# Kernel tuning notes

Hardware: AMD Instinct MI355X
Metric: run time of the kernel (lower is better)

The kernel has to match this reference:

```python
import jax, jax.numpy as jnp
import numpy as np

H = 8  # n_heads
NEG = -1e32
LN_EPS = 1e-5


def setup_inputs() -> dict:
    key = jax.random.key(0)
    ks = jax.random.split(key, 10)
    B, S, D = 8, 1024, 512
    sd = 1.0 / np.sqrt(D)
    return {
        "q_in": jax.random.normal(ks[0], (B, S, D), jnp.float32),
        "k_in": jax.random.normal(ks[1], (B, S, D), jnp.float32),
        "v_in": jax.random.normal(ks[2], (B, S, D), jnp.float32),
        "state_mask": jax.random.randint(ks[3], (B, S, S), 0, 2, jnp.int32),
        "Wq": jax.random.normal(ks[4], (D, D), jnp.float32) * sd,
        "bq": jnp.zeros((D,), jnp.float32),
        "Wv": jax.random.normal(ks[5], (D, D), jnp.float32) * sd,
        "bv": jnp.zeros((D,), jnp.float32),
        "Wo": jax.random.normal(ks[6], (D, D), jnp.float32) * sd,
        "bo": jnp.zeros((D,), jnp.float32),
        "gammas": jax.random.normal(ks[7], (H, 1, 1), jnp.float32) * 0.1,
        "ln_g": jnp.ones((D,), jnp.float32),
        "ln_b": jnp.zeros((D,), jnp.float32),
    }


def _heads(x, B, S, h, dk):
    # [B,S,D] -> [B,h,S,dk]
    return x.reshape(B, S, h, dk).transpose(0, 2, 1, 3)


def reference(q_in, k_in, v_in, state_mask, Wq, bq, Wv, bv, Wo, bo, gammas, ln_g, ln_b):
    B, S, D = q_in.shape
    dk = D // H
    # strict causal mask (tril(-1)), as in DTransformerLayer with peek_cur=False
    causal = jnp.tril(jnp.ones((S, S), bool), -1)[None, None]  # [1,1,S,S]

    # --- LrState: decay-gamma scores on RAW embeddings, scaled by sqrt(d_model) (source quirk) ---
    qh = _heads(q_in, B, S, H, dk)
    kh = _heads(k_in, B, S, H, dk)
    s_scores = jnp.einsum("bhqd,bhkd->bhqk", qh, kh) / jnp.sqrt(jnp.float32(D))
    total_effect = jnp.clip(jnp.exp(-jax.nn.softplus(gammas)), 1e-5, 1e5)[None]  # [1,H,1,1]
    s_scores = s_scores * total_effect
    new_mask = (state_mask[:, None] != 0) & causal  # cluster mask AND causal
    s_scores = jnp.where(new_mask, s_scores, 0.0)

    # --- MultiHeadAttention (kq_same=True: k uses q_linear) ---
    q = _heads(q_in @ Wq + bq, B, S, H, dk)
    k = _heads(k_in @ Wq + bq, B, S, H, dk)
    v = _heads(v_in @ Wv + bv, B, S, H, dk)
    scores = jnp.einsum("bhqd,bhkd->bhqk", q, k) / jnp.sqrt(jnp.float32(dk))
    scores = jnp.where(causal, scores, NEG)
    scores = scores + s_scores
    scores = jnp.where(causal, scores, NEG)
    probs = jax.nn.softmax(scores, axis=-1)
    probs = jnp.where(causal, probs, 0.0)
    o = jnp.einsum("bhqk,bhkd->bhqd", probs, v)
    o = o.transpose(0, 2, 1, 3).reshape(B, S, D) @ Wo + bo

    # residual (dropout inactive in eval) + LayerNorm
    x = q_in + o
    mu = jnp.mean(x, -1, keepdims=True)
    var = jnp.mean(jnp.square(x - mu), -1, keepdims=True)
    return (x - mu) * jax.lax.rsqrt(var + LN_EPS) * ln_g + ln_b
```

## Files before the change

### kernel.cpp

```cpp
#include <hip/hip_runtime.h>
#include <math.h>

#define S_LEN 1024
#define D_MOD 512
#define NH 8
#define DK 64
#define NB 8

typedef __attribute__((ext_vector_type(8))) short short8;
typedef __attribute__((ext_vector_type(4))) float floatx4;

union U8 { ushort u[8]; short8 v; };

__device__ __forceinline__ ushort f2bf(float x) {
  unsigned u = __float_as_uint(x);
  unsigned r = (u + 0x7fffu + ((u >> 16) & 1u)) >> 16;
  return (ushort)r;
}

__global__ __launch_bounds__(256) void prep_kern(
    const float* __restrict__ q, const float* __restrict__ k,
    const float* __restrict__ v, const int* __restrict__ smask,
    ushort* __restrict__ qo, ushort* __restrict__ ko,
    ushort* __restrict__ vo, unsigned long long* __restrict__ mb)
{
  const int y = blockIdx.y;
  const int t = threadIdx.x;
  if (y < 3) {
    const float* src = (y == 0) ? q : (y == 1) ? k : v;
    ushort* dst = (y == 0) ? qo : (y == 1) ? ko : vo;
    const int i = blockIdx.x * 256 + t;
    const float4 a = *((const float4*)src + i * 2);
    const float4 b = *((const float4*)src + i * 2 + 1);
    U8 o;
    o.u[0] = f2bf(a.x); o.u[1] = f2bf(a.y); o.u[2] = f2bf(a.z); o.u[3] = f2bf(a.w);
    o.u[4] = f2bf(b.x); o.u[5] = f2bf(b.y); o.u[6] = f2bf(b.z); o.u[7] = f2bf(b.w);
    *(short8*)(dst + (size_t)i * 8) = o.v;
  } else {
    const int row = blockIdx.x * 4 + (t >> 6);
    const int lane = t & 63;
    const int* p = smask + (size_t)row * S_LEN;
    unsigned long long mine = 0;
#pragma unroll
    for (int r = 0; r < 16; ++r) {
      int m = p[r * 64 + lane];
      unsigned long long w = __ballot(m != 0);
      if (lane == r) mine = w;
    }
    if (lane < 16) mb[(size_t)row * 16 + lane] = mine;
  }
}

__global__ __launch_bounds__(256) void wtrans3_kern(
    const float* __restrict__ W0, const float* __restrict__ W1,
    const float* __restrict__ W2, ushort* __restrict__ T0,
    ushort* __restrict__ T1, ushort* __restrict__ T2)
{
  const int z = blockIdx.z;
  const float* W = (z == 0) ? W0 : (z == 1) ? W1 : W2;
  ushort* Wt = (z == 0) ? T0 : (z == 1) ? T1 : T2;
  __shared__ __align__(16) ushort tile[64][72];
  const int t = threadIdx.x;
  const int n0 = blockIdx.x * 64;
  const int k0 = blockIdx.y * 64;
  {
    const int r = t >> 2;
    const int c0 = (t & 3) * 16;
    const float* p = &W[(size_t)(k0 + r) * 512 + n0 + c0];
#pragma unroll
    for (int j = 0; j < 16; ++j) tile[r][c0 + j] = f2bf(p[j]);
  }
  __syncthreads();
  {
    const int c = t >> 2;
    const int kg = (t & 3) * 16;
    U8 lo, hi;
#pragma unroll
    for (int j = 0; j < 8; ++j) lo.u[j] = tile[kg + j][c];
#pragma unroll
    for (int j = 0; j < 8; ++j) hi.u[j] = tile[kg + 8 + j][c];
    ushort* q = &Wt[(size_t)(n0 + c) * 512 + k0 + kg];
    *(short8*)q = lo.v;
    *(short8*)(q + 8) = hi.v;
  }
}

__global__ __launch_bounds__(256) void gemm_qkv_kern(
    const ushort* __restrict__ qr, const ushort* __restrict__ kr,
    const ushort* __restrict__ vr, const ushort* __restrict__ Wqt,
    const ushort* __restrict__ Wvt, const float* __restrict__ bq,
    const float* __restrict__ bv, ushort* __restrict__ Qo,
    ushort* __restrict__ Ko, ushort* __restrict__ VtO)
{
  __shared__ __align__(16) ushort Bl[2][64][64];

  const int z = blockIdx.z;
  const ushort* A = (z == 0) ? qr : (z == 1) ? kr : vr;
  const ushort* Wt = (z == 2) ? Wvt : Wqt;
  const float* bias = (z == 2) ? bv : bq;

  const int t = threadIdx.x;
  const int w = t >> 6;
  const int lane = t & 63;
  const int quad = lane >> 4;
  const int i16 = lane & 15;
  const int mbase = blockIdx.x * 128 + w * 32;
  const int nbase = blockIdx.y * 64;

  const int sr = t >> 2;
  const int slc = (t & 3) * 2;
  const int sp0 = ((slc ^ (sr & 7)) * 8);
  const int sp1 = (((slc + 1) ^ (sr & 7)) * 8);
  const ushort* Bg = Wt + (size_t)(nbase + sr) * 512 + (t & 3) * 16;
  const int xb = i16 & 7;

  const ushort* Ap = A + (size_t)(mbase + i16) * 512 + quad * 8;

  floatx4 acc[2][4];
#pragma unroll
  for (int mi = 0; mi < 2; ++mi)
#pragma unroll
    for (int ni = 0; ni < 4; ++ni) acc[mi][ni] = (floatx4)(0.f);

  short8 areg[3][2][2];
#pragma unroll
  for (int d = 0; d < 2; ++d)
#pragma unroll
    for (int mi = 0; mi < 2; ++mi)
#pragma unroll
      for (int kc = 0; kc < 2; ++kc)
        areg[d][mi][kc] = *(const short8*)(Ap + d * 64 + kc * 32 + mi * 16 * 512);

  {
    short8 b0 = *(const short8*)Bg;
    short8 b1 = *(const short8*)(Bg + 8);
    *(short8*)&Bl[0][sr][sp0] = b0;
    *(short8*)&Bl[0][sr][sp1] = b1;
    __syncthreads();
  }

#pragma unroll
  for (int kt = 0; kt < 8; ++kt) {
    const int cb = kt & 1;
    short8 nb0, nb1;
    if (kt < 7) {
      nb0 = *(const short8*)(Bg + (kt + 1) * 64);
      nb1 = *(const short8*)(Bg + (kt + 1) * 64 + 8);
    }
    if (kt < 6) {
#pragma unroll
      for (int mi = 0; mi < 2; ++mi)
#pragma unroll
        for (int kc = 0; kc < 2; ++kc)
          areg[(kt + 2) % 3][mi][kc] =
              *(const short8*)(Ap + (kt + 2) * 64 + kc * 32 + mi * 16 * 512);
    }
    short8 bf[2][4];
#pragma unroll
    for (int kc = 0; kc < 2; ++kc)
#pragma unroll
      for (int ni = 0; ni < 4; ++ni)
        bf[kc][ni] = *(const short8*)&Bl[cb][ni * 16 + i16][((kc * 4 + quad) ^ xb) * 8];
#pragma unroll
    for (int kc = 0; kc < 2; ++kc)
#pragma unroll
      for (int mi = 0; mi < 2; ++mi)
#pragma unroll
        for (int ni = 0; ni < 4; ++ni)
          acc[mi][ni] = __builtin_amdgcn_mfma_f32_16x16x32_bf16(
              areg[kt % 3][mi][kc], bf[kc][ni], acc[mi][ni], 0, 0, 0);
    if (kt < 7) {
      *(short8*)&Bl[cb ^ 1][sr][sp0] = nb0;
      *(short8*)&Bl[cb ^ 1][sr][sp1] = nb1;
      __syncthreads();
    }
  }

  float bv4[4];
#pragma unroll
  for (int ni = 0; ni < 4; ++ni) bv4[ni] = bias[nbase + ni * 16 + i16];

  if (z < 2) {
    ushort* C = (z == 0) ? Qo : Ko;
#pragma unroll
    for (int mi = 0; mi < 2; ++mi)
#pragma unroll
      for (int ni = 0; ni < 4; ++ni)
#pragma unroll
        for (int r = 0; r < 4; ++r) {
          const int m = mbase + mi * 16 + quad * 4 + r;
          const int n = nbase + ni * 16 + i16;
          C[(size_t)m * 512 + n] = f2bf(acc[mi][ni][r] + bv4[ni]);
        }
  } else {
#pragma unroll
    for (int mi = 0; mi < 2; ++mi)
#pragma unroll
      for (int ni = 0; ni < 4; ++ni) {
        const int m = mbase + mi * 16 + quad * 4;
        const int b = m >> 10;
        const int s = m & 1023;
        const int n = nbase + ni * 16 + i16;
        const int h = n >> 6;
        const int c = n & 63;
        ushort4 pk;
        pk.x = f2bf(acc[mi][ni][0] + bv4[ni]);
        pk.y = f2bf(acc[mi][ni][1] + bv4[ni]);
        pk.z = f2bf(acc[mi][ni][2] + bv4[ni]);
        pk.w = f2bf(acc[mi][ni][3] + bv4[ni]);
        *(ushort4*)(VtO + (((size_t)b * NH + h) * DK + c) * S_LEN + s) = pk;
      }
  }
}

__global__ __launch_bounds__(256) void gemm_out_kern(
    const ushort* __restrict__ A, const ushort* __restrict__ Wt,
    const float* __restrict__ bias, const float* __restrict__ R,
    float* __restrict__ X)
{
  __shared__ __align__(16) ushort Bl[2][64][64];

  const int t = threadIdx.x;
  const int w = t >> 6;
  const int lane = t & 63;
  const int quad = lane >> 4;
  const int i16 = lane & 15;
  const int mbase = blockIdx.x * 128 + w * 32;
  const int nbase = blockIdx.y * 64;

  const int sr = t >> 2;
  const int slc = (t & 3) * 2;
  const int sp0 = ((slc ^ (sr & 7)) * 8);
  const int sp1 = (((slc + 1) ^ (sr & 7)) * 8);
  const ushort* Bg = Wt + (size_t)(nbase + sr) * 512 + (t & 3) * 16;
  const int xb = i16 & 7;

  const ushort* Ap = A + (size_t)(mbase + i16) * 512 + quad * 8;

  floatx4 acc[2][4];
#pragma unroll
  for (int mi = 0; mi < 2; ++mi)
#pragma unroll
    for (int ni = 0; ni < 4; ++ni) acc[mi][ni] = (floatx4)(0.f);

  short8 areg[3][2][2];
#pragma unroll
  for (int d = 0; d < 2; ++d)
#pragma unroll
    for (int mi = 0; mi < 2; ++mi)
#pragma unroll
      for (int kc = 0; kc < 2; ++kc)
        areg[d][mi][kc] = *(const short8*)(Ap + d * 64 + kc * 32 + mi * 16 * 512);

  {
    short8 b0 = *(const short8*)Bg;
    short8 b1 = *(const short8*)(Bg + 8);
    *(short8*)&Bl[0][sr][sp0] = b0;
    *(short8*)&Bl[0][sr][sp1] = b1;
    __syncthreads();
  }

#pragma unroll
  for (int kt = 0; kt < 8; ++kt) {
    const int cb = kt & 1;
    short8 nb0, nb1;
    if (kt < 7) {
      nb0 = *(const short8*)(Bg + (kt + 1) * 64);
      nb1 = *(const short8*)(Bg + (kt + 1) * 64 + 8);
    }
    if (kt < 6) {
#pragma unroll
      for (int mi = 0; mi < 2; ++mi)
#pragma unroll
        for (int kc = 0; kc < 2; ++kc)
          areg[(kt + 2) % 3][mi][kc] =
              *(const short8*)(Ap + (kt + 2) * 64 + kc * 32 + mi * 16 * 512);
    }
    short8 bf[2][4];
#pragma unroll
    for (int kc = 0; kc < 2; ++kc)
#pragma unroll
      for (int ni = 0; ni < 4; ++ni)
        bf[kc][ni] = *(const short8*)&Bl[cb][ni * 16 + i16][((kc * 4 + quad) ^ xb) * 8];
#pragma unroll
    for (int kc = 0; kc < 2; ++kc)
#pragma unroll
      for (int mi = 0; mi < 2; ++mi)
#pragma unroll
        for (int ni = 0; ni < 4; ++ni)
          acc[mi][ni] = __builtin_amdgcn_mfma_f32_16x16x32_bf16(
              areg[kt % 3][mi][kc], bf[kc][ni], acc[mi][ni], 0, 0, 0);
    if (kt < 7) {
      *(short8*)&Bl[cb ^ 1][sr][sp0] = nb0;
      *(short8*)&Bl[cb ^ 1][sr][sp1] = nb1;
      __syncthreads();
    }
  }

  float bv4[4];
#pragma unroll
  for (int ni = 0; ni < 4; ++ni) bv4[ni] = bias[nbase + ni * 16 + i16];
#pragma unroll
  for (int mi = 0; mi < 2; ++mi)
#pragma unroll
    for (int ni = 0; ni < 4; ++ni)
#pragma unroll
      for (int r = 0; r < 4; ++r) {
        const int m = mbase + mi * 16 + quad * 4 + r;
        const int n = nbase + ni * 16 + i16;
        X[(size_t)m * 512 + n] = acc[mi][ni][r] + bv4[ni] + R[(size_t)m * 512 + n];
      }
}

__global__ __launch_bounds__(256) void attn_kern(
    const ushort* __restrict__ Qb, const ushort* __restrict__ Kb,
    const ushort* __restrict__ VtG, const ushort* __restrict__ qraw,
    const ushort* __restrict__ kraw,
    const unsigned long long* __restrict__ mbits,
    const float* __restrict__ gammas, ushort* __restrict__ Obf)
{
  __shared__ __align__(16) ushort Kp[2][64][64];
  __shared__ __align__(16) ushort Kr[2][64][64];
  __shared__ __align__(16) ushort Vc[2][64][64];
  __shared__ __align__(16) ushort Pl[4][16][64];

  const int t = threadIdx.x;
  const int w = t >> 6;
  const int lane = t & 63;
  const int quad = lane >> 4;
  const int i16 = lane & 15;
  const int bh = blockIdx.x;
  const int b = bh >> 3;
  const int h = bh & 7;
  const int p = blockIdx.y;

  const float gam = gammas[h];
  float te = __expf(-log1pf(__expf(gam)));
  te = fminf(fmaxf(te, 1e-5f), 1e5f);
  const float c1 = 0.125f * 1.44269504f;
  const float c2 = te * 0.044194173824159216f * 1.44269504f;

  const int xi = i16 & 7;
  const int rr = t >> 3;
  const int lc = t & 7;
  const int pc = ((lc ^ (rr & 7)) * 8);

  const ushort* kpgB = Kb + ((size_t)b * S_LEN + rr) * D_MOD + h * DK + lc * 8;
  const ushort* krgB = kraw + ((size_t)b * S_LEN + rr) * D_MOD + h * DK + lc * 8;
  const ushort* vgB  = VtG + ((size_t)bh * DK + rr) * S_LEN + lc * 8;

#pragma unroll
  for (int seg = 0; seg < 2; ++seg) {
    const int qt = seg ? (15 - p) : p;
    const int qbase = qt * 64 + w * 16;

    short8 Qp[2], Qr[2];
    {
      const ushort* qp = Qb + ((size_t)b * S_LEN + qbase + i16) * D_MOD + h * DK + quad * 8;
      const ushort* qq = qraw + ((size_t)b * S_LEN + qbase + i16) * D_MOD + h * DK + quad * 8;
#pragma unroll
      for (int s = 0; s < 2; ++s) {
        Qp[s] = *(const short8*)(qp + s * 32);
        Qr[s] = *(const short8*)(qq + s * 32);
      }
    }

    floatx4 Oacc[4];
#pragma unroll
    for (int t4 = 0; t4 < 4; ++t4) Oacc[t4] = (floatx4)(0.f);
    float l_run[4] = {0.f, 0.f, 0.f, 0.f};

    const int nit = qt + 1;

    {
      short8 k0v0 = *(const short8*)kpgB;
      short8 k0v1 = *(const short8*)(kpgB + 32 * D_MOD);
      short8 r0v0 = *(const short8*)krgB;
      short8 r0v1 = *(const short8*)(krgB + 32 * D_MOD);
      short8 v0v0 = *(const short8*)vgB;
      short8 v0v1 = *(const short8*)(vgB + 32 * S_LEN);
      __syncthreads();
      *(short8*)&Kp[0][rr][pc] = k0v0;
      *(short8*)&Kp[0][rr + 32][pc] = k0v1;
      *(short8*)&Kr[0][rr][pc] = r0v0;
      *(short8*)&Kr[0][rr + 32][pc] = r0v1;
      *(short8*)&Vc[0][rr][pc] = v0v0;
      *(short8*)&Vc[0][rr + 32][pc] = v0v1;
      __syncthreads();
    }

    for (int kt = 0; kt < nit; ++kt) {
      const int cb = kt & 1;
      const bool havenext = (kt + 1 < nit);
      const bool diag = (kt == qt);

      short8 nk0, nk1, nr0, nr1, nv0, nv1;
      if (havenext) {
        const size_t ko = (size_t)(kt + 1) * 64;
        nk0 = *(const short8*)(kpgB + ko * D_MOD);
        nk1 = *(const short8*)(kpgB + ko * D_MOD + 32 * D_MOD);
        nr0 = *(const short8*)(krgB + ko * D_MOD);
        nr1 = *(const short8*)(krgB + ko * D_MOD + 32 * D_MOD);
        nv0 = *(const short8*)(vgB + ko);
        nv1 = *(const short8*)(vgB + ko + 32 * S_LEN);
      }

      unsigned long long mw[4];
#pragma unroll
      for (int r = 0; r < 4; ++r)
        mw[r] = mbits[((size_t)b * S_LEN + qbase + quad * 4 + r) * 16 + kt];

      floatx4 accp[4], accr[4];
#pragma unroll
      for (int t4 = 0; t4 < 4; ++t4) { accp[t4] = (floatx4)(0.f); accr[t4] = (floatx4)(0.f); }
#pragma unroll
      for (int s = 0; s < 2; ++s) {
        const int co = ((s * 4 + quad) ^ xi) * 8;
        short8 kp4[4], kr4[4];
#pragma unroll
        for (int t4 = 0; t4 < 4; ++t4) kp4[t4] = *(const short8*)&Kp[cb][t4 * 16 + i16][co];
#pragma unroll
        for (int t4 = 0; t4 < 4; ++t4) kr4[t4] = *(const short8*)&Kr[cb][t4 * 16 + i16][co];
#pragma unroll
        for (int t4 = 0; t4 < 4; ++t4)
          accp[t4] = __builtin_amdgcn_mfma_f32_16x16x32_bf16(Qp[s], kp4[t4], accp[t4], 0, 0, 0);
#pragma unroll
        for (int t4 = 0; t4 < 4; ++t4)
          accr[t4] = __builtin_amdgcn_mfma_f32_16x16x32_bf16(Qr[s], kr4[t4], accr[t4], 0, 0, 0);
      }

      const int k0g = kt * 64;
#pragma unroll
      for (int r = 0; r < 4; ++r) {
        const int qg = qbase + quad * 4 + r;
        const int prow = quad * 4 + r;
#pragma unroll
        for (int t4 = 0; t4 < 4; ++t4) {
          const float bitf = ((mw[r] >> (t4 * 16 + i16)) & 1ULL) ? c2 : 0.f;
          const float sv = accp[t4][r] * c1 + accr[t4][r] * bitf;
          float pv = __builtin_amdgcn_exp2f(sv);
          if (diag) {
            const int kg = k0g + t4 * 16 + i16;
            pv = (kg < qg) ? pv : 0.f;
          }
          l_run[r] += pv;
          const int kc = t4 * 2 + (i16 >> 3);
          Pl[w][prow][((kc ^ (prow & 7)) * 8) + (i16 & 7)] =
              (ushort)(__float_as_uint(pv) >> 16);
        }
      }

#pragma unroll
      for (int s = 0; s < 2; ++s) {
        const int co = ((s * 4 + quad) ^ xi) * 8;
        short8 a = *(const short8*)&Pl[w][i16][co];
#pragma unroll
        for (int t4 = 0; t4 < 4; ++t4) {
          short8 bv8 = *(const short8*)&Vc[cb][t4 * 16 + i16][co];
          Oacc[t4] = __builtin_amdgcn_mfma_f32_16x16x32_bf16(a, bv8, Oacc[t4], 0, 0, 0);
        }
      }

      if (havenext) {
        *(short8*)&Kp[cb ^ 1][rr][pc] = nk0;
        *(short8*)&Kp[cb ^ 1][rr + 32][pc] = nk1;
        *(short8*)&Kr[cb ^ 1][rr][pc] = nr0;
        *(short8*)&Kr[cb ^ 1][rr + 32][pc] = nr1;
        *(short8*)&Vc[cb ^ 1][rr][pc] = nv0;
        *(short8*)&Vc[cb ^ 1][rr + 32][pc] = nv1;
        __syncthreads();
      }
    }

#pragma unroll
    for (int r = 0; r < 4; ++r) {
      float l = l_run[r];
#pragma unroll
      for (int off = 1; off < 16; off <<= 1) l += __shfl_xor(l, off);
      const float inv = (l > 0.f) ? 1.f / l : 0.f;
      ushort* orow = Obf + ((size_t)b * S_LEN + qbase + quad * 4 + r) * D_MOD + h * DK;
#pragma unroll
      for (int t4 = 0; t4 < 4; ++t4)
        orow[t4 * 16 + i16] = f2bf(Oacc[t4][r] * inv);
    }
  }
}

__global__ __launch_bounds__(256) void ln_kern(
    const float* __restrict__ X, const float* __restrict__ gw,
    const float* __restrict__ bw, float* __restrict__ out)
{
  const int row = blockIdx.x * 4 + (threadIdx.x >> 6);
  const int lane = threadIdx.x & 63;
  const int c = lane * 8;
  const float* xp = &X[(size_t)row * D_MOD + c];
  const float4 x0 = *(const float4*)xp;
  const float4 x1 = *(const float4*)(xp + 4);
  float xv[8] = {x0.x, x0.y, x0.z, x0.w, x1.x, x1.y, x1.z, x1.w};
  float sum = 0.f;
#pragma unroll
  for (int u = 0; u < 8; ++u) sum += xv[u];
#pragma unroll
  for (int off = 1; off < 64; off <<= 1) sum += __shfl_xor(sum, off, 64);
  const float mu = sum * (1.f / 512.f);
  float ss = 0.f;
#pragma unroll
  for (int u = 0; u < 8; ++u) { xv[u] -= mu; ss += xv[u] * xv[u]; }
#pragma unroll
  for (int off = 1; off < 64; off <<= 1) ss += __shfl_xor(ss, off, 64);
  const float rstd = rsqrtf(ss * (1.f / 512.f) + 1e-5f);
  const float4 g0 = *(const float4*)&gw[c];
  const float4 g1 = *(const float4*)&gw[c + 4];
  const float4 b0 = *(const float4*)&bw[c];
  const float4 b1 = *(const float4*)&bw[c + 4];
  float* op = &out[(size_t)row * D_MOD + c];
  *(float4*)op = make_float4(xv[0] * rstd * g0.x + b0.x,
                             xv[1] * rstd * g0.y + b0.y,
                             xv[2] * rstd * g0.z + b0.z,
                             xv[3] * rstd * g0.w + b0.w);
  *(float4*)(op + 4) = make_float4(xv[4] * rstd * g1.x + b1.x,
                                   xv[5] * rstd * g1.y + b1.y,
                                   xv[6] * rstd * g1.z + b1.z,
                                   xv[7] * rstd * g1.w + b1.w);
}

extern "C" void kernel_launch(void* const* d_in, const int* in_sizes, int n_in,
                              void* d_out, int out_size, void* d_ws, size_t ws_size,
                              hipStream_t stream)
{
  const float* q_in  = (const float*)d_in[0];
  const float* k_in  = (const float*)d_in[1];
  const float* v_in  = (const float*)d_in[2];
  const int*   smask = (const int*)d_in[3];
  const float* Wq = (const float*)d_in[4];
  const float* bq = (const float*)d_in[5];
  const float* Wv = (const float*)d_in[6];
  const float* bv = (const float*)d_in[7];
  const float* Wo = (const float*)d_in[8];
  const float* bo = (const float*)d_in[9];
  const float* gammas = (const float*)d_in[10];
  const float* ln_g = (const float*)d_in[11];
  const float* ln_b = (const float*)d_in[12];
  float* out = (float*)d_out;

  char* ws = (char*)d_ws;
  const size_t BF = (size_t)NB * S_LEN * D_MOD * sizeof(ushort);
  ushort* qr  = (ushort*)(ws);
  ushort* kr  = (ushort*)(ws + BF);
  ushort* vr  = (ushort*)(ws + 2 * BF);
  ushort* Obf = (ushort*)(ws + 2 * BF);
  ushort* Qbf = (ushort*)(ws + 3 * BF);
  ushort* Kbf = (ushort*)(ws + 4 * BF);
  ushort* Vt  = (ushort*)(ws + 5 * BF);
  unsigned long long* mbits = (unsigned long long*)(ws + 6 * BF);
  ushort* Wqt = (ushort*)(ws + 6 * BF + (1 << 20));
  ushort* Wvt = Wqt + 512 * 512;
  ushort* Wot = Wvt + 512 * 512;
  float*  X   = (float*)ws;

  const dim3 tb(256);

  prep_kern<<<dim3(2048, 4), tb, 0, stream>>>(q_in, k_in, v_in, smask,
                                              qr, kr, vr, mbits);
  wtrans3_kern<<<dim3(8, 8, 3), tb, 0, stream>>>(Wq, Wv, Wo, Wqt, Wvt, Wot);

  gemm_qkv_kern<<<dim3(64, 8, 3), tb, 0, stream>>>(qr, kr, vr, Wqt, Wvt,
                                                   bq, bv, Qbf, Kbf, Vt);

  attn_kern<<<dim3(64, 8), tb, 0, stream>>>(Qbf, Kbf, Vt, qr, kr, mbits,
                                            gammas, Obf);

  gemm_out_kern<<<dim3(64, 8), tb, 0, stream>>>(Obf, Wot, bo, q_in, X);
  ln_kern<<<2048, tb, 0, stream>>>(X, ln_g, ln_b, out);
}
```

Measured before the change: 231.2 us.

## Restructure attention to 32x32 MFMA with 2-wave blocks and fold weight transpose into prep

The attention kernel now uses 128-thread blocks where each wave handles 32 query rows. It computes the two score products with 32x32x16 bf16 MFMA in transposed (K x Q) form, which puts one query per lane, loads a single mask word per tile, and lets P be written as packed 4-element stores. The softmax scale factor is folded into the Q projection epilogue, and the weight-transpose kernel is merged into the prep kernel as an extra grid row, saving one launch. The tradeoffs are half as many waves per block and higher register pressure from the 16-wide accumulators.

```diff
diff --git a/kernel.cpp b/kernel.cpp
--- a/kernel.cpp
+++ b/kernel.cpp
@@ -9,6 +9,7 @@
 
 typedef __attribute__((ext_vector_type(8))) short short8;
 typedef __attribute__((ext_vector_type(4))) float floatx4;
+typedef __attribute__((ext_vector_type(16))) float floatx16;
 
 union U8 { ushort u[8]; short8 v; };
 
@@ -18,12 +19,18 @@
   return (ushort)r;
 }
 
+#define SC1 0.18033688f
+
 __global__ __launch_bounds__(256) void prep_kern(
     const float* __restrict__ q, const float* __restrict__ k,
     const float* __restrict__ v, const int* __restrict__ smask,
-    ushort* __restrict__ qo, ushort* __restrict__ ko,
-    ushort* __restrict__ vo, unsigned long long* __restrict__ mb)
+    const float* __restrict__ W0, const float* __restrict__ W1,
+    const float* __restrict__ W2,
+    ushort* __restrict__ qo, ushort* __restrict__ ko, ushort* __restrict__ vo,
+    unsigned long long* __restrict__ mb,
+    ushort* __restrict__ T0, ushort* __restrict__ T1, ushort* __restrict__ T2)
 {
+  __shared__ __align__(16) ushort tile[64][72];
   const int y = blockIdx.y;
   const int t = threadIdx.x;
   if (y < 3) {
@@ -36,7 +43,7 @@
     o.u[0] = f2bf(a.x); o.u[1] = f2bf(a.y); o.u[2] = f2bf(a.z); o.u[3] = f2bf(a.w);
     o.u[4] = f2bf(b.x); o.u[5] = f2bf(b.y); o.u[6] = f2bf(b.z); o.u[7] = f2bf(b.w);
     *(short8*)(dst + (size_t)i * 8) = o.v;
-  } else {
+  } else if (y == 3) {
     const int row = blockIdx.x * 4 + (t >> 6);
     const int lane = t & 63;
     const int* p = smask + (size_t)row * S_LEN;
@@ -48,40 +55,34 @@
       if (lane == r) mine = w;
     }
     if (lane < 16) mb[(size_t)row * 16 + lane] = mine;
-  }
-}
-
-__global__ __launch_bounds__(256) void wtrans3_kern(
-    const float* __restrict__ W0, const float* __restrict__ W1,
-    const float* __restrict__ W2, ushort* __restrict__ T0,
-    ushort* __restrict__ T1, ushort* __restrict__ T2)
-{
-  const int z = blockIdx.z;
-  const float* W = (z == 0) ? W0 : (z == 1) ? W1 : W2;
-  ushort* Wt = (z == 0) ? T0 : (z == 1) ? T1 : T2;
-  __shared__ __align__(16) ushort tile[64][72];
-  const int t = threadIdx.x;
-  const int n0 = blockIdx.x * 64;
-  const int k0 = blockIdx.y * 64;
-  {
-    const int r = t >> 2;
-    const int c0 = (t & 3) * 16;
-    const float* p = &W[(size_t)(k0 + r) * 512 + n0 + c0];
-#pragma unroll
-    for (int j = 0; j < 16; ++j) tile[r][c0 + j] = f2bf(p[j]);
-  }
-  __syncthreads();
-  {
-    const int c = t >> 2;
-    const int kg = (t & 3) * 16;
-    U8 lo, hi;
-#pragma unroll
-    for (int j = 0; j < 8; ++j) lo.u[j] = tile[kg + j][c];
-#pragma unroll
-    for (int j = 0; j < 8; ++j) hi.u[j] = tile[kg + 8 + j][c];
-    ushort* q = &Wt[(size_t)(n0 + c) * 512 + k0 + kg];
-    *(short8*)q = lo.v;
-    *(short8*)(q + 8) = hi.v;
+  } else {
+    if (blockIdx.x >= 192) return;
+    const int z = blockIdx.x / 64;
+    const int xy = blockIdx.x & 63;
+    const float* W = (z == 0) ? W0 : (z == 1) ? W1 : W2;
+    ushort* Wt = (z == 0) ? T0 : (z == 1) ? T1 : T2;
+    const int n0 = (xy & 7) * 64;
+    const int k0 = (xy >> 3) * 64;
+    {
+      const int r = t >> 2;
+      const int c0 = (t & 3) * 16;
+      const float* p = &W[(size_t)(k0 + r) * 512 + n0 + c0];
+#pragma unroll
+      for (int j = 0; j < 16; ++j) tile[r][c0 + j] = f2bf(p[j]);
+    }
+    __syncthreads();
+    {
+      const int c = t >> 2;
+      const int kg = (t & 3) * 16;
+      U8 lo, hi;
+#pragma unroll
+      for (int j = 0; j < 8; ++j) lo.u[j] = tile[kg + j][c];
+#pragma unroll
+      for (int j = 0; j < 8; ++j) hi.u[j] = tile[kg + 8 + j][c];
+      ushort* qd = &Wt[(size_t)(n0 + c) * 512 + k0 + kg];
+      *(short8*)qd = lo.v;
+      *(short8*)(qd + 8) = hi.v;
+    }
   }
 }
 
@@ -182,6 +183,7 @@
 
   if (z < 2) {
     ushort* C = (z == 0) ? Qo : Ko;
+    const float sc = (z == 0) ? SC1 : 1.f;
 #pragma unroll
     for (int mi = 0; mi < 2; ++mi)
 #pragma unroll
@@ -190,7 +192,7 @@
         for (int r = 0; r < 4; ++r) {
           const int m = mbase + mi * 16 + quad * 4 + r;
           const int n = nbase + ni * 16 + i16;
-          C[(size_t)m * 512 + n] = f2bf(acc[mi][ni][r] + bv4[ni]);
+          C[(size_t)m * 512 + n] = f2bf((acc[mi][ni][r] + bv4[ni]) * sc);
         }
   } else {
 #pragma unroll
@@ -312,7 +314,7 @@
       }
 }
 
-__global__ __launch_bounds__(256) void attn_kern(
+__global__ __launch_bounds__(128) void attn_kern(
     const ushort* __restrict__ Qb, const ushort* __restrict__ Kb,
     const ushort* __restrict__ VtG, const ushort* __restrict__ qraw,
     const ushort* __restrict__ kraw,
@@ -322,12 +324,14 @@
   __shared__ __align__(16) ushort Kp[2][64][64];
   __shared__ __align__(16) ushort Kr[2][64][64];
   __shared__ __align__(16) ushort Vc[2][64][64];
-  __shared__ __align__(16) ushort Pl[4][16][64];
+  __shared__ __align__(16) ushort Pl[2][32][64];
 
   const int t = threadIdx.x;
   const int w = t >> 6;
   const int lane = t & 63;
-  const int quad = lane >> 4;
+  const int l31 = lane & 31;
+  const int lh = lane >> 5;
+  const int quad = (lane >> 4) & 3;
   const int i16 = lane & 15;
   const int bh = blockIdx.x;
   const int b = bh >> 3;
@@ -337,55 +341,57 @@
   const float gam = gammas[h];
   float te = __expf(-log1pf(__expf(gam)));
   te = fminf(fmaxf(te, 1e-5f), 1e5f);
-  const float c1 = 0.125f * 1.44269504f;
   const float c2 = te * 0.044194173824159216f * 1.44269504f;
 
-  const int xi = i16 & 7;
-  const int rr = t >> 3;
+  const int rr4 = t >> 3;
   const int lc = t & 7;
-  const int pc = ((lc ^ (rr & 7)) * 8);
-
-  const ushort* kpgB = Kb + ((size_t)b * S_LEN + rr) * D_MOD + h * DK + lc * 8;
-  const ushort* krgB = kraw + ((size_t)b * S_LEN + rr) * D_MOD + h * DK + lc * 8;
-  const ushort* vgB  = VtG + ((size_t)bh * DK + rr) * S_LEN + lc * 8;
+  const int pc = ((lc ^ (rr4 & 7)) * 8);
+  const ushort* kpgB = Kb + ((size_t)b * S_LEN + rr4) * D_MOD + h * DK + lc * 8;
+  const ushort* krgB = kraw + ((size_t)b * S_LEN + rr4) * D_MOD + h * DK + lc * 8;
+  const ushort* vgB  = VtG + ((size_t)bh * DK + rr4) * S_LEN + lc * 8;
 
 #pragma unroll
   for (int seg = 0; seg < 2; ++seg) {
     const int qt = seg ? (15 - p) : p;
-    const int qbase = qt * 64 + w * 16;
-
-    short8 Qp[2], Qr[2];
+    const int qbase = qt * 64 + w * 32;
+    const int qg = qbase + l31;
+
+    short8 Qp[4], Qr[4];
     {
-      const ushort* qp = Qb + ((size_t)b * S_LEN + qbase + i16) * D_MOD + h * DK + quad * 8;
-      const ushort* qq = qraw + ((size_t)b * S_LEN + qbase + i16) * D_MOD + h * DK + quad * 8;
-#pragma unroll
-      for (int s = 0; s < 2; ++s) {
-        Qp[s] = *(const short8*)(qp + s * 32);
-        Qr[s] = *(const short8*)(qq + s * 32);
-      }
-    }
-
-    floatx4 Oacc[4];
-#pragma unroll
-    for (int t4 = 0; t4 < 4; ++t4) Oacc[t4] = (floatx4)(0.f);
-    float l_run[4] = {0.f, 0.f, 0.f, 0.f};
+      const ushort* qp = Qb + ((size_t)b * S_LEN + qg) * D_MOD + h * DK + lh * 8;
+      const ushort* qq = qraw + ((size_t)b * S_LEN + qg) * D_MOD + h * DK + lh * 8;
+#pragma unroll
+      for (int ds = 0; ds < 4; ++ds) {
+        Qp[ds] = *(const short8*)(qp + ds * 16);
+        Qr[ds] = *(const short8*)(qq + ds * 16);
+      }
+    }
+    const unsigned long long* mrow = mbits + ((size_t)b * S_LEN + qg) * 16;
+
+    floatx4 Oacc[2][4];
+#pragma unroll
+    for (int sub = 0; sub < 2; ++sub)
+#pragma unroll
+      for (int t4 = 0; t4 < 4; ++t4) Oacc[sub][t4] = (floatx4)(0.f);
+    float l_run = 0.f;
 
     const int nit = qt + 1;
 
     {
-      short8 k0v0 = *(const short8*)kpgB;
-      short8 k0v1 = *(const short8*)(kpgB + 32 * D_MOD);
-      short8 r0v0 = *(const short8*)krgB;
-      short8 r0v1 = *(const short8*)(krgB + 32 * D_MOD);
-      short8 v0v0 = *(const short8*)vgB;
-      short8 v0v1 = *(const short8*)(vgB + 32 * S_LEN);
+      short8 kv[4], rv[4], vv[4];
+#pragma unroll
+      for (int u = 0; u < 4; ++u) {
+        kv[u] = *(const short8*)(kpgB + (size_t)(16 * u) * D_MOD);
+        rv[u] = *(const short8*)(krgB + (size_t)(16 * u) * D_MOD);
+        vv[u] = *(const short8*)(vgB + (size_t)(16 * u) * S_LEN);
+      }
       __syncthreads();
-      *(short8*)&Kp[0][rr][pc] = k0v0;
-      *(short8*)&Kp[0][rr + 32][pc] = k0v1;
-      *(short8*)&Kr[0][rr][pc] = r0v0;
-      *(short8*)&Kr[0][rr + 32][pc] = r0v1;
-      *(short8*)&Vc[0][rr][pc] = v0v0;
-      *(short8*)&Vc[0][rr + 32][pc] = v0v1;
+#pragma unroll
+      for (int u = 0; u < 4; ++u) {
+        *(short8*)&Kp[0][rr4 + 16 * u][pc] = kv[u];
+        *(short8*)&Kr[0][rr4 + 16 * u][pc] = rv[u];
+        *(short8*)&Vc[0][rr4 + 16 * u][pc] = vv[u];
+      }
       __syncthreads();
     }
 
@@ -393,96 +399,105 @@
       const int cb = kt & 1;
       const bool havenext = (kt + 1 < nit);
       const bool diag = (kt == qt);
-
-      short8 nk0, nk1, nr0, nr1, nv0, nv1;
+      const int k0 = kt * 64;
+
+      short8 nk[4], nr[4], nv[4];
       if (havenext) {
-        const size_t ko = (size_t)(kt + 1) * 64;
-        nk0 = *(const short8*)(kpgB + ko * D_MOD);
-        nk1 = *(const short8*)(kpgB + ko * D_MOD + 32 * D_MOD);
-        nr0 = *(const short8*)(krgB + ko * D_MOD);
-        nr1 = *(const short8*)(krgB + ko * D_MOD + 32 * D_MOD);
-        nv0 = *(const short8*)(vgB + ko);
-        nv1 = *(const short8*)(vgB + ko + 32 * S_LEN);
-      }
-
-      unsigned long long mw[4];
-#pragma unroll
-      for (int r = 0; r < 4; ++r)
-        mw[r] = mbits[((size_t)b * S_LEN + qbase + quad * 4 + r) * 16 + kt];
-
-      floatx4 accp[4], accr[4];
-#pragma unroll
-      for (int t4 = 0; t4 < 4; ++t4) { accp[t4] = (floatx4)(0.f); accr[t4] = (floatx4)(0.f); }
-#pragma unroll
-      for (int s = 0; s < 2; ++s) {
-        const int co = ((s * 4 + quad) ^ xi) * 8;
-        short8 kp4[4], kr4[4];
-#pragma unroll
-        for (int t4 = 0; t4 < 4; ++t4) kp4[t4] = *(const short8*)&Kp[cb][t4 * 16 + i16][co];
-#pragma unroll
-        for (int t4 = 0; t4 < 4; ++t4) kr4[t4] = *(const short8*)&Kr[cb][t4 * 16 + i16][co];
+        const size_t ko = (size_t)(k0 + 64);
+#pragma unroll
+        for (int u = 0; u < 4; ++u) {
+          nk[u] = *(const short8*)(kpgB + (ko + 16 * u) * D_MOD);
+          nr[u] = *(const short8*)(krgB + (ko + 16 * u) * D_MOD);
+          nv[u] = *(const short8*)(vgB + ko + (size_t)(16 * u) * S_LEN);
+        }
+      }
+      const unsigned long long mw = mrow[kt];
+      const unsigned mwl = (unsigned)mw;
+      const unsigned mwh = (unsigned)(mw >> 32);
+
+      floatx16 accp[2], accr[2];
+#pragma unroll
+      for (int ct = 0; ct < 2; ++ct) { accp[ct] = (floatx16)(0.f); accr[ct] = (floatx16)(0.f); }
+      const int xk = l31 & 7;
+#pragma unroll
+      for (int ds = 0; ds < 4; ++ds) {
+        const int co = ((ds * 2 + lh) ^ xk) * 8;
+        short8 kpf0 = *(const short8*)&Kp[cb][l31][co];
+        short8 kpf1 = *(const short8*)&Kp[cb][32 + l31][co];
+        short8 krf0 = *(const short8*)&Kr[cb][l31][co];
+        short8 krf1 = *(const short8*)&Kr[cb][32 + l31][co];
+        accp[0] = __builtin_amdgcn_mfma_f32_32x32x16_bf16(kpf0, Qp[ds], accp[0], 0, 0, 0);
+        accp[1] = __builtin_amdgcn_mfma_f32_32x32x16_bf16(kpf1, Qp[ds], accp[1], 0, 0, 0);
+        accr[0] = __builtin_amdgcn_mfma_f32_32x32x16_bf16(krf0, Qr[ds], accr[0], 0, 0, 0);
+        accr[1] = __builtin_amdgcn_mfma_f32_32x32x16_bf16(krf1, Qr[ds], accr[1], 0, 0, 0);
+      }
+
+#pragma unroll
+      for (int ct = 0; ct < 2; ++ct) {
+        const unsigned mh = ct ? mwh : mwl;
+#pragma unroll
+        for (int j = 0; j < 4; ++j) {
+          float pv4[4];
+#pragma unroll
+          for (int rr = 0; rr < 4; ++rr) {
+            const int r = j * 4 + rr;
+            const int key_local = rr + 4 * lh + 8 * j;
+            const float bitf = ((mh >> key_local) & 1u) ? c2 : 0.f;
+            const float sv = accp[ct][r] + accr[ct][r] * bitf;
+            float pv = __builtin_amdgcn_exp2f(sv);
+            if (diag) {
+              const int kg = k0 + ct * 32 + key_local;
+              pv = (kg < qg) ? pv : 0.f;
+            }
+            l_run += pv;
+            pv4[rr] = pv;
+          }
+          unsigned u0 = (__float_as_uint(pv4[1]) & 0xffff0000u) |
+                        (__float_as_uint(pv4[0]) >> 16);
+          unsigned u1 = (__float_as_uint(pv4[3]) & 0xffff0000u) |
+                        (__float_as_uint(pv4[2]) >> 16);
+          uint2 pk = make_uint2(u0, u1);
+          *(uint2*)&Pl[w][l31][((ct * 4 + j) ^ xk) * 8 + 4 * lh] = pk;
+        }
+      }
+
+#pragma unroll
+      for (int sub = 0; sub < 2; ++sub)
+#pragma unroll
+        for (int s = 0; s < 2; ++s) {
+          const int arow = sub * 16 + i16;
+          short8 a = *(const short8*)&Pl[w][arow][((s * 4 + quad) ^ (i16 & 7)) * 8];
+#pragma unroll
+          for (int t4 = 0; t4 < 4; ++t4) {
+            short8 bv8 = *(const short8*)&Vc[cb][t4 * 16 + i16][((s * 4 + quad) ^ (i16 & 7)) * 8];
+            Oacc[sub][t4] = __builtin_amdgcn_mfma_f32_16x16x32_bf16(a, bv8, Oacc[sub][t4], 0, 0, 0);
+          }
+        }
+
+      if (havenext) {
+#pragma unroll
+        for (int u = 0; u < 4; ++u) {
+          *(short8*)&Kp[cb ^ 1][rr4 + 16 * u][pc] = nk[u];
+          *(short8*)&Kr[cb ^ 1][rr4 + 16 * u][pc] = nr[u];
+          *(short8*)&Vc[cb ^ 1][rr4 + 16 * u][pc] = nv[u];
+        }
+        __syncthreads();
+      }
+    }
+
+    const float l_tot = l_run + __shfl_xor(l_run, 32);
+#pragma unroll
+    for (int sub = 0; sub < 2; ++sub)
+#pragma unroll
+      for (int r = 0; r < 4; ++r) {
+        const int q_local = sub * 16 + quad * 4 + r;
+        const float lq = __shfl(l_tot, q_local);
+        const float inv = (lq > 0.f) ? 1.f / lq : 0.f;
+        ushort* orow = Obf + ((size_t)b * S_LEN + qbase + q_local) * D_MOD + h * DK;
 #pragma unroll
         for (int t4 = 0; t4 < 4; ++t4)
-          accp[t4] = __builtin_amdgcn_mfma_f32_16x16x32_bf16(Qp[s], kp4[t4], accp[t4], 0, 0, 0);
-#pragma unroll
-        for (int t4 = 0; t4 < 4; ++t4)
-          accr[t4] = __builtin_amdgcn_mfma_f32_16x16x32_bf16(Qr[s], kr4[t4], accr[t4], 0, 0, 0);
-      }
-
-      const int k0g = kt * 64;
-#pragma unroll
-      for (int r = 0; r < 4; ++r) {
-        const int qg = qbase + quad * 4 + r;
-        const int prow = quad * 4 + r;
-#pragma unroll
-        for (int t4 = 0; t4 < 4; ++t4) {
-          const float bitf = ((mw[r] >> (t4 * 16 + i16)) & 1ULL) ? c2 : 0.f;
-          const float sv = accp[t4][r] * c1 + accr[t4][r] * bitf;
-          float pv = __builtin_amdgcn_exp2f(sv);
-          if (diag) {
-            const int kg = k0g + t4 * 16 + i16;
-            pv = (kg < qg) ? pv : 0.f;
-          }
-          l_run[r] += pv;
-          const int kc = t4 * 2 + (i16 >> 3);
-          Pl[w][prow][((kc ^ (prow & 7)) * 8) + (i16 & 7)] =
-              (ushort)(__float_as_uint(pv) >> 16);
-        }
-      }
-
-#pragma unroll
-      for (int s = 0; s < 2; ++s) {
-        const int co = ((s * 4 + quad) ^ xi) * 8;
-        short8 a = *(const short8*)&Pl[w][i16][co];
-#pragma unroll
-        for (int t4 = 0; t4 < 4; ++t4) {
-          short8 bv8 = *(const short8*)&Vc[cb][t4 * 16 + i16][co];
-          Oacc[t4] = __builtin_amdgcn_mfma_f32_16x16x32_bf16(a, bv8, Oacc[t4], 0, 0, 0);
-        }
-      }
-
-      if (havenext) {
-        *(short8*)&Kp[cb ^ 1][rr][pc] = nk0;
-        *(short8*)&Kp[cb ^ 1][rr + 32][pc] = nk1;
-        *(short8*)&Kr[cb ^ 1][rr][pc] = nr0;
-        *(short8*)&Kr[cb ^ 1][rr + 32][pc] = nr1;
-        *(short8*)&Vc[cb ^ 1][rr][pc] = nv0;
-        *(short8*)&Vc[cb ^ 1][rr + 32][pc] = nv1;
-        __syncthreads();
-      }
-    }
-
-#pragma unroll
-    for (int r = 0; r < 4; ++r) {
-      float l = l_run[r];
-#pragma unroll
-      for (int off = 1; off < 16; off <<= 1) l += __shfl_xor(l, off);
-      const float inv = (l > 0.f) ? 1.f / l : 0.f;
-      ushort* orow = Obf + ((size_t)b * S_LEN + qbase + quad * 4 + r) * D_MOD + h * DK;
-#pragma unroll
-      for (int t4 = 0; t4 < 4; ++t4)
-        orow[t4 * 16 + i16] = f2bf(Oacc[t4][r] * inv);
-    }
+          orow[t4 * 16 + i16] = f2bf(Oacc[sub][t4][r] * inv);
+      }
   }
 }
 
@@ -560,15 +575,16 @@
 
   const dim3 tb(256);
 
-  prep_kern<<<dim3(2048, 4), tb, 0, stream>>>(q_in, k_in, v_in, smask,
-                                              qr, kr, vr, mbits);
-  wtrans3_kern<<<dim3(8, 8, 3), tb, 0, stream>>>(Wq, Wv, Wo, Wqt, Wvt, Wot);
+  prep_kern<<<dim3(2048, 5), tb, 0, stream>>>(q_in, k_in, v_in, smask,
+                                              Wq, Wv, Wo,
+                                              qr, kr, vr, mbits,
+                                              Wqt, Wvt, Wot);
 
   gemm_qkv_kern<<<dim3(64, 8, 3), tb, 0, stream>>>(qr, kr, vr, Wqt, Wvt,
                                                    bq, bv, Qbf, Kbf, Vt);
 
-  attn_kern<<<dim3(64, 8), tb, 0, stream>>>(Qbf, Kbf, Vt, qr, kr, mbits,
-                                            gammas, Obf);
+  attn_kern<<<dim3(64, 8), dim3(128), 0, stream>>>(Qbf, Kbf, Vt, qr, kr, mbits,
+                                                   gammas, Obf);
 
   gemm_out_kern<<<dim3(64, 8), tb, 0, stream>>>(Obf, Wot, bo, q_in, X);
   ln_kern<<<2048, tb, 0, stream>>>(X, ln_g, ln_b, out);
```

Measured after the change: 235.2 us. Within noise of the previous version (+1.7%).
